# Optimization experiments

Hardware: AMD Instinct MI355X
Metric: run time of the kernel (lower is better)

## Reference

```python
import jax, jax.numpy as jnp
import numpy as np

B, T = 128, 512
H = 64          # hidden_dim
E = 64          # input_embed_dim
H4 = 4 * H


def _block_mask(in_dim, out_dim):
    # DroppedLinearV2 mask: 4 diagonal blocks, shape (4*in_dim, 4*out_dim)
    m = np.zeros((4 * in_dim, 4 * out_dim), dtype=np.float32)
    for i in range(4):
        m[i * in_dim:(i + 1) * in_dim, i * out_dim:(i + 1) * out_dim] = 1.0
    return jnp.asarray(m)


def setup_inputs() -> dict:
    key = jax.random.key(0)
    ks = jax.random.split(key, 16)
    s = 0.05
    return {
        "event": jax.random.randint(ks[0], (B, T), 0, 4),
        "time_step": jax.random.uniform(ks[1], (B, T), dtype=jnp.float32),
        "mkt_state": jax.random.randint(ks[2], (B, T), 0, 3),
        # type embedding MLP: Linear(4,E), Tanh, Linear(E,E), Tanh
        "et_W1": jax.random.normal(ks[3], (E, 4), dtype=jnp.float32) * s,
        "et_b1": jnp.zeros((E,), jnp.float32),
        "et_W2": jax.random.normal(ks[4], (E, E), dtype=jnp.float32) * s,
        "et_b2": jnp.zeros((E,), jnp.float32),
        # state embedding MLP: Linear(3,E), Tanh, Linear(E,E), Tanh
        "es_W1": jax.random.normal(ks[5], (E, 3), dtype=jnp.float32) * s,
        "es_b1": jnp.zeros((E,), jnp.float32),
        "es_W2": jax.random.normal(ks[6], (E, E), dtype=jnp.float32) * s,
        "es_b2": jnp.zeros((E,), jnp.float32),
        # 7 gates: [input_g, forget_g, output_g, input_target, forget_target, z_gate, decay]
        "g_W1": jax.random.normal(ks[7], (7, H4, E + H4), dtype=jnp.float32) * s,
        "g_b1": jnp.zeros((7, H4), jnp.float32),
        "g_W2": jax.random.normal(ks[8], (7, H4, H4), dtype=jnp.float32) * s,
        "g_b2": jnp.zeros((7, H4), jnp.float32),
        # intensity layer: DroppedLinearV2(H, 1) -> weight (4, 4H)
        "i_W": jax.random.normal(ks[9], (4, H4), dtype=jnp.float32) * s,
        "i_b": jnp.zeros((4,), jnp.float32),
    }


def _forward(event, time_step, mkt_state, et_W1, et_b1, et_W2, et_b2,
             es_W1, es_b1, es_W2, es_b2, g_W1, g_b1, g_W2, g_b2, i_W, i_b):
    seq_len = event.shape[1]
    # embeddings (mkt_state=True path): x = type_embedding + state_embedding
    oh_e = jax.nn.one_hot(event, 4, dtype=jnp.float32)
    te = jnp.tanh(jnp.tanh(oh_e @ et_W1.T + et_b1) @ et_W2.T + et_b2)
    oh_s = jax.nn.one_hot(mkt_state, 3, dtype=jnp.float32)
    se = jnp.tanh(jnp.tanh(oh_s @ es_W1.T + es_b1) @ es_W2.T + es_b2)
    x = te + se                                   # [B, T, E]

    gmask = _block_mask(H, H)                     # (4H, 4H)
    g_W2m = g_W2 * gmask.T[None]                  # effective masked gate weights
    i_Wm = i_W * _block_mask(H, 1).T              # (4, 4H)

    x_seq = jnp.swapaxes(x[:, :seq_len - 1], 0, 1)   # [T-1, B, E]
    dt_seq = time_step[:, 1:].T                      # [T-1, B]

    def step(carry, inp):
        h, c, ct = carry
        x_t, dt = inp
        v = jnp.concatenate([x_t, h], axis=1)                      # [B, E+4H]
        pre = jnp.tanh(jnp.einsum('bi,kgi->bkg', v, g_W1) + g_b1)  # [B,7,4H]
        g = jnp.einsum('bkg,kog->bko', pre, g_W2m) + g_b2          # [B,7,4H]
        inpt = jax.nn.sigmoid(g[:, 0])
        forget = jax.nn.sigmoid(g[:, 1])
        outp = jax.nn.sigmoid(g[:, 2])
        in_tg = jax.nn.sigmoid(g[:, 3])
        fg_tg = jax.nn.sigmoid(g[:, 4])
        z = jnp.tanh(g[:, 5])
        decay = jax.nn.softplus(g[:, 6])
        c_i = forget * c + inpt * z
        ct_new = fg_tg * ct + in_tg * z
        c_new = ct_new + (c_i - ct_new) * jnp.exp(-decay * dt[:, None])
        h_new = outp * jnp.tanh(c_new)
        return (h_new, c_new, ct_new), (c_i, ct_new, outp, decay, h_new)

    zero = jnp.zeros((event.shape[0], H4), jnp.float32)
    _, (cells, cell_targets, outputs, decays, h_all) = jax.lax.scan(
        step, (zero, zero, zero), (x_seq, dt_seq))

    intens = jax.nn.softplus(jnp.einsum('tbg,og->tbo', h_all, i_Wm) + i_b)
    tr = lambda a: jnp.swapaxes(a, 0, 1)  # [T-1,B,.] -> [B,T-1,.]
    return (tr(intens), tr(cells), tr(cell_targets), tr(outputs), tr(decays))


def reference(event, time_step, mkt_state, et_W1, et_b1, et_W2, et_b2,
              es_W1, es_b1, es_W2, es_b2, g_W1, g_b1, g_W2, g_b2, i_W, i_b):
    return _forward(event, time_step, mkt_state, et_W1, et_b1, et_W2, et_b2,
                    es_W1, es_b1, es_W2, es_b2, g_W1, g_b1, g_W2, g_b2, i_W, i_b)
```

## Files before the change

### kernel.cpp

```cpp
#include <hip/hip_runtime.h>
#include <stdint.h>

typedef unsigned short u16;
typedef unsigned char u8;
typedef unsigned long long u64;
typedef short s16x8 __attribute__((ext_vector_type(8)));
typedef float f32x4 __attribute__((ext_vector_type(4)));
typedef float f32x2 __attribute__((ext_vector_type(2)));
typedef unsigned int u32x4 __attribute__((ext_vector_type(4)));
typedef unsigned int u32x2 __attribute__((ext_vector_type(2)));

#define NB 128
#define NT 512
#define NH 256
#define GQ 8
#define MBQ 16
#define STEPS 511

#define WS_HBUF 0
#define WS_X12  131072
#define WS_BAR  134144

#define OFF_H     0
#define OFF_PRE   8448
#define OFF_G     24576
#define OFF_XC    55040
#define OFF_B2    78336
#define OFF_IW    80128
#define OFF_X12   80384
#define OFF_IDXA  83456
#define OFF_DTA   91648
#define SMEM_BYTES 124416

__device__ __forceinline__ u16 f2bf(float f) {
  unsigned u = __float_as_uint(f);
  u += 0x7FFFu + ((u >> 16) & 1u);
  return (u16)(u >> 16);
}
__device__ __forceinline__ float sigm(float x) { return 1.0f / (1.0f + __expf(-x)); }
__device__ __forceinline__ float tanh_fast(float x) {
  float e = __expf(2.0f * x);
  return 1.0f - 2.0f / (e + 1.0f);
}
__device__ __forceinline__ float softplus_f(float x) {
  return fmaxf(x, 0.0f) + __logf(1.0f + __expf(-fabsf(x)));
}

__global__ void ct4_prep(const float* __restrict__ etW1, const float* __restrict__ etb1,
                         const float* __restrict__ etW2, const float* __restrict__ etb2,
                         const float* __restrict__ esW1, const float* __restrict__ esb1,
                         const float* __restrict__ esW2, const float* __restrict__ esb2,
                         char* __restrict__ ws) {
  __shared__ float sT[4][64];
  __shared__ float sS[3][64];
  const int i = threadIdx.x;
  #pragma unroll
  for (int e = 0; e < 4; ++e) sT[e][i] = tanhf(etW1[i * 4 + e] + etb1[i]);
  #pragma unroll
  for (int s = 0; s < 3; ++s) sS[s][i] = tanhf(esW1[i * 3 + s] + esb1[i]);
  __syncthreads();
  float te[4], se[3];
  #pragma unroll
  for (int e = 0; e < 4; ++e) {
    float a = etb2[i];
    for (int jj = 0; jj < 64; ++jj) a += sT[e][jj] * etW2[i * 64 + jj];
    te[e] = tanhf(a);
  }
  #pragma unroll
  for (int s = 0; s < 3; ++s) {
    float a = esb2[i];
    for (int jj = 0; jj < 64; ++jj) a += sS[s][jj] * esW2[i * 64 + jj];
    se[s] = tanhf(a);
  }
  float* x12 = (float*)(ws + WS_X12);
  #pragma unroll
  for (int e = 0; e < 4; ++e)
    #pragma unroll
    for (int s = 0; s < 3; ++s) x12[(e * 3 + s) * 64 + i] = te[e] + se[s];
  u32x4* hz = (u32x4*)(ws + WS_HBUF);
  u32x4 z = {0u, 0u, 0u, 0u};
  for (int p = i; p < 65536 / 16; p += 64) hz[p] = z;
  int* bars = (int*)(ws + WS_BAR);
  for (int p = i; p < 1024; p += 64) bars[p] = 0;
}

__global__ __launch_bounds__(512, 1) void ct4_main(
    const int* __restrict__ ev, const float* __restrict__ ts, const int* __restrict__ mk,
    const float* __restrict__ gW1, const float* __restrict__ gb1,
    const float* __restrict__ gW2, const float* __restrict__ gb2,
    const float* __restrict__ iW, const float* __restrict__ ibp,
    float* __restrict__ out, char* __restrict__ ws) {
  extern __shared__ char smem[];
  u16* h_lds = (u16*)(smem + OFF_H);
  float* g_lds = (float*)(smem + OFF_G);
  float* xc_lds = (float*)(smem + OFF_XC);
  float* b2_lds = (float*)(smem + OFF_B2);
  float* iw_lds = (float*)(smem + OFF_IW);
  float* x12_lds = (float*)(smem + OFF_X12);
  u8* idx_all = (u8*)(smem + OFF_IDXA);
  float* dt_all = (float*)(smem + OFF_DTA);

  const int tid = threadIdx.x;
  const int bid = blockIdx.x;
  const int grp = bid & 7;
  const int j = bid >> 3;
  const int b0 = grp * MBQ;
  const int wave = tid >> 6;
  const int q = (tid >> 4) & 3;
  const int c = tid & 15;
  const int kloc0 = 2 * j;

  u16* hbuf = (u16*)(ws + WS_HBUF);
  int* bars = (int*)(ws + WS_BAR);
  int* myflag = bars + grp * 128 + j * 32;

  for (int p = tid; p < 12 * 64; p += 512) x12_lds[p] = ((const float*)(ws + WS_X12))[p];
  for (int p = tid; p < 16 * 264 / 2; p += 512) ((unsigned*)h_lds)[p] = 0u;
  if (tid < 448) {
    int kk = tid >> 6, o = tid & 63;
    b2_lds[kk * 64 + o] = gb2[kk * 256 + j * 64 + o];
  }
  if (tid < 64) iw_lds[tid] = iW[j * 256 + j * 64 + tid];
  const float ibj = ibp[j];
  for (int p = tid; p < STEPS * 16; p += 512) {
    int t = p >> 4, b = p & 15;
    idx_all[p] = (u8)(ev[(b0 + b) * NT + t] * 3 + mk[(b0 + b) * NT + t]);
    dt_all[p] = ts[(b0 + b) * NT + t + 1];
  }
  __syncthreads();
  if (tid < 448) {
    int kk = tid >> 6, o = tid & 63;
    const float* row = gW1 + (size_t)(kk * 256 + j * 64 + o) * 320;
    float a[12];
    float bb = gb1[kk * 256 + j * 64 + o];
    #pragma unroll
    for (int m = 0; m < 12; ++m) a[m] = bb;
    for (int i = 0; i < 64; ++i) {
      float w = row[i];
      #pragma unroll
      for (int m = 0; m < 12; ++m) a[m] += x12_lds[m * 64 + i] * w;
    }
    #pragma unroll
    for (int m = 0; m < 12; ++m) xc_lds[(kk * 64 + o) * 13 + m] = a[m];
  }

  s16x8 a1[4][8];
  s16x8 a2[4][2];
  const int k = wave;
  if (wave < 7) {
    #pragma unroll
    for (int s = 0; s < 8; ++s) {
      int kt = (s < 6) ? (s + (s >= kloc0 ? 2 : 0)) : (kloc0 + (s - 6));
      #pragma unroll
      for (int mt = 0; mt < 4; ++mt) {
        const float* p = gW1 + (size_t)(k * 256 + j * 64 + 16 * mt + c) * 320 + 64 + 32 * kt + 8 * q;
        union { s16x8 v; u16 u[8]; } fr;
        #pragma unroll
        for (int i = 0; i < 8; ++i) fr.u[i] = f2bf(p[i]);
        a1[mt][s] = fr.v;
      }
    }
    #pragma unroll
    for (int mt = 0; mt < 4; ++mt)
      #pragma unroll
      for (int kt = 0; kt < 2; ++kt) {
        const float* p = gW2 + (size_t)(k * 256 + j * 64 + 16 * mt + c) * 256 + j * 64 + 32 * kt + 8 * q;
        union { s16x8 v; u16 u[8]; } fr;
        #pragma unroll
        for (int i = 0; i < 8; ++i) fr.u[i] = f2bf(p[i]);
        a2[mt][kt] = fr.v;
      }
  }

  float ccA[2] = {0.f, 0.f};
  float cctA[2] = {0.f, 0.f};
  f32x4 acc[4] = {};
  const f32x4 fzero = {};
  __syncthreads();

  const int O_CELL = NB * STEPS * 4;
  const int SZB = NB * STEPS * NH;
  const int O_CT = O_CELL + SZB;
  const int O_OUT = O_CT + SZB;
  const int O_DEC = O_OUT + SZB;

  for (int t = 0; t < STEPS; ++t) {
    if (wave < 7) {
      #pragma unroll
      for (int s = 0; s < 6; ++s) {
        int ks = s + (s >= kloc0 ? 2 : 0);
        s16x8 bf = *(const s16x8*)&h_lds[c * 264 + 32 * ks + 8 * q];
        #pragma unroll
        for (int mt = 0; mt < 4; ++mt)
          acc[mt] = __builtin_amdgcn_mfma_f32_16x16x32_bf16(a1[mt][s], bf, acc[mt], 0, 0, 0);
      }
      u16* preW = (u16*)(smem + OFF_PRE) + k * (16 * 72);
      int midx = (int)idx_all[t * 16 + c];
      #pragma unroll
      for (int mt = 0; mt < 4; ++mt) {
        int o = 16 * mt + 4 * q;
        const float* xr = &xc_lds[(k * 64 + o) * 13 + midx];
        u16 u0 = f2bf(tanh_fast(acc[mt][0] + xr[0]));
        u16 u1 = f2bf(tanh_fast(acc[mt][1] + xr[13]));
        u16 u2 = f2bf(tanh_fast(acc[mt][2] + xr[26]));
        u16 u3 = f2bf(tanh_fast(acc[mt][3] + xr[39]));
        u32x2 pk;
        pk[0] = (unsigned)u0 | ((unsigned)u1 << 16);
        pk[1] = (unsigned)u2 | ((unsigned)u3 << 16);
        *(u32x2*)&preW[c * 72 + o] = pk;
      }
      f32x4 acc2[4] = {};
      #pragma unroll
      for (int kt = 0; kt < 2; ++kt) {
        s16x8 pf = *(const s16x8*)&preW[c * 72 + 32 * kt + 8 * q];
        #pragma unroll
        for (int mt = 0; mt < 4; ++mt)
          acc2[mt] = __builtin_amdgcn_mfma_f32_16x16x32_bf16(a2[mt][kt], pf, acc2[mt], 0, 0, 0);
      }
      #pragma unroll
      for (int mt = 0; mt < 4; ++mt)
        *(f32x4*)&g_lds[(k * 16 + c) * 68 + 16 * mt + 4 * q] = acc2[mt];
    }
    __syncthreads();

    const int b = tid >> 5, o2 = (tid & 31) * 2;
    float ip = 0.f;
    float ci[2], ctn[2], opv[2], dcv[2];
    {
      float dtv = dt_all[t * 16 + b];
      float G[7][2];
      #pragma unroll
      for (int kk = 0; kk < 7; ++kk) {
        f32x2 gg = *(const f32x2*)&g_lds[(kk * 16 + b) * 68 + o2];
        G[kk][0] = gg[0] + b2_lds[kk * 64 + o2];
        G[kk][1] = gg[1] + b2_lds[kk * 64 + o2 + 1];
      }
      float hnv[2];
      #pragma unroll
      for (int e = 0; e < 2; ++e) {
        float inp = sigm(G[0][e]);
        float fg = sigm(G[1][e]);
        float op = sigm(G[2][e]);
        float itg = sigm(G[3][e]);
        float ftg = sigm(G[4][e]);
        float z = tanh_fast(G[5][e]);
        float dc = softplus_f(G[6][e]);
        float c_i = fg * ccA[e] + inp * z;
        float c_t = ftg * cctA[e] + itg * z;
        float edv = __expf(-dc * dtv);
        float c_n = c_t + (c_i - c_t) * edv;
        float h_n = op * tanh_fast(c_n);
        ccA[e] = c_n;
        cctA[e] = c_t;
        ci[e] = c_i; ctn[e] = c_t; opv[e] = op; dcv[e] = dc;
        hnv[e] = h_n;
        ip += iw_lds[o2 + e] * h_n;
      }
      unsigned hp = (unsigned)f2bf(hnv[0]) | ((unsigned)f2bf(hnv[1]) << 16);
      if (t < STEPS - 1) {
        *(unsigned*)&h_lds[b * 264 + j * 64 + o2] = hp;
        __hip_atomic_store((unsigned*)&hbuf[((size_t)(((t + 1) & 1) * GQ + grp) * MBQ + b) * 256 + j * 64 + o2],
                           hp, __ATOMIC_RELAXED, __HIP_MEMORY_SCOPE_AGENT);
      }
    }
    __syncthreads();

    auto C2 = [&]() {
      size_t base = ((size_t)(b0 + b) * STEPS + t) * NH + j * 64 + o2;
      f32x2 v;
      v[0] = ci[0];  v[1] = ci[1];  __builtin_nontemporal_store(v, (f32x2*)&out[O_CELL + base]);
      v[0] = ctn[0]; v[1] = ctn[1]; __builtin_nontemporal_store(v, (f32x2*)&out[O_CT + base]);
      v[0] = opv[0]; v[1] = opv[1]; __builtin_nontemporal_store(v, (f32x2*)&out[O_OUT + base]);
      v[0] = dcv[0]; v[1] = dcv[1]; __builtin_nontemporal_store(v, (f32x2*)&out[O_DEC + base]);
      #pragma unroll
      for (int d = 1; d < 32; d <<= 1) ip += __shfl_xor(ip, d, 32);
      if ((tid & 31) == 0)
        __builtin_nontemporal_store(softplus_f(ip + ibj),
                                    &out[((size_t)(b0 + b) * STEPS + t) * 4 + j]);
    };

    if (t < STEPS - 1) {
      if (tid == 0) __hip_atomic_store(myflag, t + 1, __ATOMIC_RELAXED, __HIP_MEMORY_SCOPE_AGENT);
      if (wave < 7) {
        #pragma unroll
        for (int mt = 0; mt < 4; ++mt) acc[mt] = fzero;
        #pragma unroll
        for (int s = 6; s < 8; ++s) {
          int ks = kloc0 + (s - 6);
          s16x8 bf = *(const s16x8*)&h_lds[c * 264 + 32 * ks + 8 * q];
          #pragma unroll
          for (int mt = 0; mt < 4; ++mt)
            acc[mt] = __builtin_amdgcn_mfma_f32_16x16x32_bf16(a1[mt][s], bf, acc[mt], 0, 0, 0);
        }
        C2();
      } else {
        C2();
        const int l = tid & 63;
        const int row = l >> 2;
        const int segb = (l & 3) * 32;
        int* f0p = bars + grp * 128 + (0 + (0 >= j)) * 32;
        int* f1p = bars + grp * 128 + (1 + (1 >= j)) * 32;
        int* f2p = bars + grp * 128 + (2 + (2 >= j)) * 32;
        for (;;) {
          int f0 = __hip_atomic_load(f0p, __ATOMIC_RELAXED, __HIP_MEMORY_SCOPE_AGENT);
          int f1 = __hip_atomic_load(f1p, __ATOMIC_RELAXED, __HIP_MEMORY_SCOPE_AGENT);
          int f2 = __hip_atomic_load(f2p, __ATOMIC_RELAXED, __HIP_MEMORY_SCOPE_AGENT);
          if (f0 > t && f1 > t && f2 > t) break;
          __builtin_amdgcn_s_sleep(1);
        }
        const char* rbase = (const char*)hbuf +
            ((size_t)(((t + 1) & 1) * GQ + grp) * MBQ + row) * 512 + segb;
        u64 dv[3][4];
        #pragma unroll
        for (int rb = 0; rb < 3; ++rb) {
          int jr = rb + (rb >= j);
          const u64* src = (const u64*)(rbase + jr * 128);
          #pragma unroll
          for (int kq = 0; kq < 4; ++kq)
            dv[rb][kq] = __hip_atomic_load(src + kq, __ATOMIC_RELAXED, __HIP_MEMORY_SCOPE_AGENT);
        }
        char* lbase = (char*)h_lds + row * 528 + segb;
        #pragma unroll
        for (int rb = 0; rb < 3; ++rb) {
          int jr = rb + (rb >= j);
          #pragma unroll
          for (int kq = 0; kq < 4; ++kq)
            *(u64*)(lbase + jr * 128 + 8 * kq) = dv[rb][kq];
        }
      }
      __syncthreads();
    } else {
      C2();
    }
  }
}

extern "C" void kernel_launch(void* const* d_in, const int* in_sizes, int n_in,
                              void* d_out, int out_size, void* d_ws, size_t ws_size,
                              hipStream_t stream) {
  const int* ev = (const int*)d_in[0];
  const float* ts = (const float*)d_in[1];
  const int* mk = (const int*)d_in[2];
  const float* etW1 = (const float*)d_in[3];
  const float* etb1 = (const float*)d_in[4];
  const float* etW2 = (const float*)d_in[5];
  const float* etb2 = (const float*)d_in[6];
  const float* esW1 = (const float*)d_in[7];
  const float* esb1 = (const float*)d_in[8];
  const float* esW2 = (const float*)d_in[9];
  const float* esb2 = (const float*)d_in[10];
  const float* gW1 = (const float*)d_in[11];
  const float* gb1 = (const float*)d_in[12];
  const float* gW2 = (const float*)d_in[13];
  const float* gb2 = (const float*)d_in[14];
  const float* iW = (const float*)d_in[15];
  const float* ibv = (const float*)d_in[16];
  char* ws = (char*)d_ws;
  float* out = (float*)d_out;

  ct4_prep<<<1, 64, 0, stream>>>(etW1, etb1, etW2, etb2, esW1, esb1, esW2, esb2, ws);
  (void)hipFuncSetAttribute((const void*)ct4_main,
                            hipFuncAttributeMaxDynamicSharedMemorySize, SMEM_BYTES);
  ct4_main<<<GQ * 4, 512, SMEM_BYTES, stream>>>(ev, ts, mk, gW1, gb1, gW2, gb2, iW, ibv, out, ws);
}
```

Measured before the change: 2.230 ms.

## Halve block to 256 threads, each wave computing two gates

The main kernel drops from 8 waves to 4 per block. Each wave now holds the bf16 weight fragments for two of the seven gates, reusing one set of h-fragment loads for both gates' MFMAs. The elementwise cell update handles 4 hidden units per thread and writes wider vector stores, and wave 3 now does the cross-block polling and gather. This cuts block-wide barrier cost and redundant LDS reads, but doubles per-wave register pressure for weights and serialises two gates' MFMA chains per wave.

```diff
diff --git a/kernel.cpp b/kernel.cpp
--- a/kernel.cpp
+++ b/kernel.cpp
@@ -84,7 +84,7 @@
   for (int p = i; p < 1024; p += 64) bars[p] = 0;
 }
 
-__global__ __launch_bounds__(512, 1) void ct4_main(
+__global__ __launch_bounds__(256, 1) void ct4_main(
     const int* __restrict__ ev, const float* __restrict__ ts, const int* __restrict__ mk,
     const float* __restrict__ gW1, const float* __restrict__ gb1,
     const float* __restrict__ gW2, const float* __restrict__ gb2,
@@ -114,22 +114,22 @@
   int* bars = (int*)(ws + WS_BAR);
   int* myflag = bars + grp * 128 + j * 32;
 
-  for (int p = tid; p < 12 * 64; p += 512) x12_lds[p] = ((const float*)(ws + WS_X12))[p];
-  for (int p = tid; p < 16 * 264 / 2; p += 512) ((unsigned*)h_lds)[p] = 0u;
-  if (tid < 448) {
-    int kk = tid >> 6, o = tid & 63;
+  for (int p = tid; p < 12 * 64; p += 256) x12_lds[p] = ((const float*)(ws + WS_X12))[p];
+  for (int p = tid; p < 16 * 264 / 2; p += 256) ((unsigned*)h_lds)[p] = 0u;
+  for (int p = tid; p < 448; p += 256) {
+    int kk = p >> 6, o = p & 63;
     b2_lds[kk * 64 + o] = gb2[kk * 256 + j * 64 + o];
   }
   if (tid < 64) iw_lds[tid] = iW[j * 256 + j * 64 + tid];
   const float ibj = ibp[j];
-  for (int p = tid; p < STEPS * 16; p += 512) {
+  for (int p = tid; p < STEPS * 16; p += 256) {
     int t = p >> 4, b = p & 15;
     idx_all[p] = (u8)(ev[(b0 + b) * NT + t] * 3 + mk[(b0 + b) * NT + t]);
     dt_all[p] = ts[(b0 + b) * NT + t + 1];
   }
   __syncthreads();
-  if (tid < 448) {
-    int kk = tid >> 6, o = tid & 63;
+  for (int r = tid; r < 448; r += 256) {
+    int kk = r >> 6, o = r & 63;
     const float* row = gW1 + (size_t)(kk * 256 + j * 64 + o) * 320;
     float a[12];
     float bb = gb1[kk * 256 + j * 64 + o];
@@ -144,37 +144,40 @@
     for (int m = 0; m < 12; ++m) xc_lds[(kk * 64 + o) * 13 + m] = a[m];
   }
 
-  s16x8 a1[4][8];
-  s16x8 a2[4][2];
-  const int k = wave;
-  if (wave < 7) {
-    #pragma unroll
-    for (int s = 0; s < 8; ++s) {
-      int kt = (s < 6) ? (s + (s >= kloc0 ? 2 : 0)) : (kloc0 + (s - 6));
-      #pragma unroll
-      for (int mt = 0; mt < 4; ++mt) {
-        const float* p = gW1 + (size_t)(k * 256 + j * 64 + 16 * mt + c) * 320 + 64 + 32 * kt + 8 * q;
-        union { s16x8 v; u16 u[8]; } fr;
-        #pragma unroll
-        for (int i = 0; i < 8; ++i) fr.u[i] = f2bf(p[i]);
-        a1[mt][s] = fr.v;
-      }
-    }
-    #pragma unroll
-    for (int mt = 0; mt < 4; ++mt)
-      #pragma unroll
-      for (int kt = 0; kt < 2; ++kt) {
-        const float* p = gW2 + (size_t)(k * 256 + j * 64 + 16 * mt + c) * 256 + j * 64 + 32 * kt + 8 * q;
-        union { s16x8 v; u16 u[8]; } fr;
-        #pragma unroll
-        for (int i = 0; i < 8; ++i) fr.u[i] = f2bf(p[i]);
-        a2[mt][kt] = fr.v;
-      }
-  }
-
-  float ccA[2] = {0.f, 0.f};
-  float cctA[2] = {0.f, 0.f};
-  f32x4 acc[4] = {};
+  s16x8 a1[2][4][8];
+  s16x8 a2[2][4][2];
+  #pragma unroll
+  for (int gg = 0; gg < 2; ++gg) {
+    const int k = 2 * wave + gg;
+    if (k < 7) {
+      #pragma unroll
+      for (int s = 0; s < 8; ++s) {
+        int kt = (s < 6) ? (s + (s >= kloc0 ? 2 : 0)) : (kloc0 + (s - 6));
+        #pragma unroll
+        for (int mt = 0; mt < 4; ++mt) {
+          const float* p = gW1 + (size_t)(k * 256 + j * 64 + 16 * mt + c) * 320 + 64 + 32 * kt + 8 * q;
+          union { s16x8 v; u16 u[8]; } fr;
+          #pragma unroll
+          for (int i = 0; i < 8; ++i) fr.u[i] = f2bf(p[i]);
+          a1[gg][mt][s] = fr.v;
+        }
+      }
+      #pragma unroll
+      for (int mt = 0; mt < 4; ++mt)
+        #pragma unroll
+        for (int kt = 0; kt < 2; ++kt) {
+          const float* p = gW2 + (size_t)(k * 256 + j * 64 + 16 * mt + c) * 256 + j * 64 + 32 * kt + 8 * q;
+          union { s16x8 v; u16 u[8]; } fr;
+          #pragma unroll
+          for (int i = 0; i < 8; ++i) fr.u[i] = f2bf(p[i]);
+          a2[gg][mt][kt] = fr.v;
+        }
+    }
+  }
+
+  float ccA[4] = {0.f, 0.f, 0.f, 0.f};
+  float cctA[4] = {0.f, 0.f, 0.f, 0.f};
+  f32x4 acc[2][4] = {};
   const f32x4 fzero = {};
   __syncthreads();
 
@@ -185,59 +188,68 @@
   const int O_DEC = O_OUT + SZB;
 
   for (int t = 0; t < STEPS; ++t) {
-    if (wave < 7) {
+    {
+      s16x8 bfr[6];
       #pragma unroll
       for (int s = 0; s < 6; ++s) {
         int ks = s + (s >= kloc0 ? 2 : 0);
-        s16x8 bf = *(const s16x8*)&h_lds[c * 264 + 32 * ks + 8 * q];
-        #pragma unroll
-        for (int mt = 0; mt < 4; ++mt)
-          acc[mt] = __builtin_amdgcn_mfma_f32_16x16x32_bf16(a1[mt][s], bf, acc[mt], 0, 0, 0);
-      }
-      u16* preW = (u16*)(smem + OFF_PRE) + k * (16 * 72);
+        bfr[s] = *(const s16x8*)&h_lds[c * 264 + 32 * ks + 8 * q];
+      }
       int midx = (int)idx_all[t * 16 + c];
       #pragma unroll
-      for (int mt = 0; mt < 4; ++mt) {
-        int o = 16 * mt + 4 * q;
-        const float* xr = &xc_lds[(k * 64 + o) * 13 + midx];
-        u16 u0 = f2bf(tanh_fast(acc[mt][0] + xr[0]));
-        u16 u1 = f2bf(tanh_fast(acc[mt][1] + xr[13]));
-        u16 u2 = f2bf(tanh_fast(acc[mt][2] + xr[26]));
-        u16 u3 = f2bf(tanh_fast(acc[mt][3] + xr[39]));
-        u32x2 pk;
-        pk[0] = (unsigned)u0 | ((unsigned)u1 << 16);
-        pk[1] = (unsigned)u2 | ((unsigned)u3 << 16);
-        *(u32x2*)&preW[c * 72 + o] = pk;
-      }
-      f32x4 acc2[4] = {};
-      #pragma unroll
-      for (int kt = 0; kt < 2; ++kt) {
-        s16x8 pf = *(const s16x8*)&preW[c * 72 + 32 * kt + 8 * q];
-        #pragma unroll
-        for (int mt = 0; mt < 4; ++mt)
-          acc2[mt] = __builtin_amdgcn_mfma_f32_16x16x32_bf16(a2[mt][kt], pf, acc2[mt], 0, 0, 0);
-      }
-      #pragma unroll
-      for (int mt = 0; mt < 4; ++mt)
-        *(f32x4*)&g_lds[(k * 16 + c) * 68 + 16 * mt + 4 * q] = acc2[mt];
+      for (int gg = 0; gg < 2; ++gg) {
+        const int k = 2 * wave + gg;
+        if (k < 7) {
+          #pragma unroll
+          for (int s = 0; s < 6; ++s)
+            #pragma unroll
+            for (int mt = 0; mt < 4; ++mt)
+              acc[gg][mt] = __builtin_amdgcn_mfma_f32_16x16x32_bf16(a1[gg][mt][s], bfr[s], acc[gg][mt], 0, 0, 0);
+          u16* preW = (u16*)(smem + OFF_PRE) + k * (16 * 72);
+          #pragma unroll
+          for (int mt = 0; mt < 4; ++mt) {
+            int o = 16 * mt + 4 * q;
+            const float* xr = &xc_lds[(k * 64 + o) * 13 + midx];
+            u16 u0 = f2bf(tanh_fast(acc[gg][mt][0] + xr[0]));
+            u16 u1 = f2bf(tanh_fast(acc[gg][mt][1] + xr[13]));
+            u16 u2 = f2bf(tanh_fast(acc[gg][mt][2] + xr[26]));
+            u16 u3 = f2bf(tanh_fast(acc[gg][mt][3] + xr[39]));
+            u32x2 pk;
+            pk[0] = (unsigned)u0 | ((unsigned)u1 << 16);
+            pk[1] = (unsigned)u2 | ((unsigned)u3 << 16);
+            *(u32x2*)&preW[c * 72 + o] = pk;
+          }
+          f32x4 acc2[4] = {};
+          #pragma unroll
+          for (int kt = 0; kt < 2; ++kt) {
+            s16x8 pf = *(const s16x8*)&preW[c * 72 + 32 * kt + 8 * q];
+            #pragma unroll
+            for (int mt = 0; mt < 4; ++mt)
+              acc2[mt] = __builtin_amdgcn_mfma_f32_16x16x32_bf16(a2[gg][mt][kt], pf, acc2[mt], 0, 0, 0);
+          }
+          #pragma unroll
+          for (int mt = 0; mt < 4; ++mt)
+            *(f32x4*)&g_lds[(k * 16 + c) * 68 + 16 * mt + 4 * q] = acc2[mt];
+        }
+      }
     }
     __syncthreads();
 
-    const int b = tid >> 5, o2 = (tid & 31) * 2;
+    const int b = tid >> 4, o4 = (tid & 15) * 4;
     float ip = 0.f;
-    float ci[2], ctn[2], opv[2], dcv[2];
+    float ci[4], ctn[4], opv[4], dcv[4];
     {
       float dtv = dt_all[t * 16 + b];
-      float G[7][2];
+      float G[7][4];
       #pragma unroll
       for (int kk = 0; kk < 7; ++kk) {
-        f32x2 gg = *(const f32x2*)&g_lds[(kk * 16 + b) * 68 + o2];
-        G[kk][0] = gg[0] + b2_lds[kk * 64 + o2];
-        G[kk][1] = gg[1] + b2_lds[kk * 64 + o2 + 1];
-      }
-      float hnv[2];
-      #pragma unroll
-      for (int e = 0; e < 2; ++e) {
+        f32x4 gg4 = *(const f32x4*)&g_lds[(kk * 16 + b) * 68 + o4];
+        #pragma unroll
+        for (int e = 0; e < 4; ++e) G[kk][e] = gg4[e] + b2_lds[kk * 64 + o4 + e];
+      }
+      float hnv[4];
+      #pragma unroll
+      for (int e = 0; e < 4; ++e) {
         float inp = sigm(G[0][e]);
         float fg = sigm(G[1][e]);
         float op = sigm(G[2][e]);
@@ -254,47 +266,63 @@
         cctA[e] = c_t;
         ci[e] = c_i; ctn[e] = c_t; opv[e] = op; dcv[e] = dc;
         hnv[e] = h_n;
-        ip += iw_lds[o2 + e] * h_n;
-      }
-      unsigned hp = (unsigned)f2bf(hnv[0]) | ((unsigned)f2bf(hnv[1]) << 16);
+        ip += iw_lds[o4 + e] * h_n;
+      }
       if (t < STEPS - 1) {
-        *(unsigned*)&h_lds[b * 264 + j * 64 + o2] = hp;
-        __hip_atomic_store((unsigned*)&hbuf[((size_t)(((t + 1) & 1) * GQ + grp) * MBQ + b) * 256 + j * 64 + o2],
+        u64 hp = (u64)f2bf(hnv[0]) | ((u64)f2bf(hnv[1]) << 16) |
+                 ((u64)f2bf(hnv[2]) << 32) | ((u64)f2bf(hnv[3]) << 48);
+        *(u64*)&h_lds[b * 264 + j * 64 + o4] = hp;
+        __hip_atomic_store((u64*)&hbuf[((size_t)(((t + 1) & 1) * GQ + grp) * MBQ + b) * 256 + j * 64 + o4],
                            hp, __ATOMIC_RELAXED, __HIP_MEMORY_SCOPE_AGENT);
       }
     }
     __syncthreads();
 
     auto C2 = [&]() {
-      size_t base = ((size_t)(b0 + b) * STEPS + t) * NH + j * 64 + o2;
-      f32x2 v;
-      v[0] = ci[0];  v[1] = ci[1];  __builtin_nontemporal_store(v, (f32x2*)&out[O_CELL + base]);
-      v[0] = ctn[0]; v[1] = ctn[1]; __builtin_nontemporal_store(v, (f32x2*)&out[O_CT + base]);
-      v[0] = opv[0]; v[1] = opv[1]; __builtin_nontemporal_store(v, (f32x2*)&out[O_OUT + base]);
-      v[0] = dcv[0]; v[1] = dcv[1]; __builtin_nontemporal_store(v, (f32x2*)&out[O_DEC + base]);
-      #pragma unroll
-      for (int d = 1; d < 32; d <<= 1) ip += __shfl_xor(ip, d, 32);
-      if ((tid & 31) == 0)
+      size_t base = ((size_t)(b0 + b) * STEPS + t) * NH + j * 64 + o4;
+      f32x4 v;
+      #pragma unroll
+      for (int e = 0; e < 4; ++e) v[e] = ci[e];
+      __builtin_nontemporal_store(v, (f32x4*)&out[O_CELL + base]);
+      #pragma unroll
+      for (int e = 0; e < 4; ++e) v[e] = ctn[e];
+      __builtin_nontemporal_store(v, (f32x4*)&out[O_CT + base]);
+      #pragma unroll
+      for (int e = 0; e < 4; ++e) v[e] = opv[e];
+      __builtin_nontemporal_store(v, (f32x4*)&out[O_OUT + base]);
+      #pragma unroll
+      for (int e = 0; e < 4; ++e) v[e] = dcv[e];
+      __builtin_nontemporal_store(v, (f32x4*)&out[O_DEC + base]);
+      #pragma unroll
+      for (int d = 1; d < 16; d <<= 1) ip += __shfl_xor(ip, d, 16);
+      if ((tid & 15) == 0)
         __builtin_nontemporal_store(softplus_f(ip + ibj),
                                     &out[((size_t)(b0 + b) * STEPS + t) * 4 + j]);
     };
 
     if (t < STEPS - 1) {
       if (tid == 0) __hip_atomic_store(myflag, t + 1, __ATOMIC_RELAXED, __HIP_MEMORY_SCOPE_AGENT);
-      if (wave < 7) {
-        #pragma unroll
-        for (int mt = 0; mt < 4; ++mt) acc[mt] = fzero;
-        #pragma unroll
-        for (int s = 6; s < 8; ++s) {
-          int ks = kloc0 + (s - 6);
-          s16x8 bf = *(const s16x8*)&h_lds[c * 264 + 32 * ks + 8 * q];
-          #pragma unroll
-          for (int mt = 0; mt < 4; ++mt)
-            acc[mt] = __builtin_amdgcn_mfma_f32_16x16x32_bf16(a1[mt][s], bf, acc[mt], 0, 0, 0);
-        }
-        C2();
-      } else {
-        C2();
+      {
+        s16x8 bfl[2];
+        #pragma unroll
+        for (int sl = 0; sl < 2; ++sl)
+          bfl[sl] = *(const s16x8*)&h_lds[c * 264 + 32 * (kloc0 + sl) + 8 * q];
+        #pragma unroll
+        for (int gg = 0; gg < 2; ++gg) {
+          const int k = 2 * wave + gg;
+          if (k < 7) {
+            #pragma unroll
+            for (int mt = 0; mt < 4; ++mt) acc[gg][mt] = fzero;
+            #pragma unroll
+            for (int sl = 0; sl < 2; ++sl)
+              #pragma unroll
+              for (int mt = 0; mt < 4; ++mt)
+                acc[gg][mt] = __builtin_amdgcn_mfma_f32_16x16x32_bf16(a1[gg][mt][6 + sl], bfl[sl], acc[gg][mt], 0, 0, 0);
+          }
+        }
+      }
+      C2();
+      if (wave == 3) {
         const int l = tid & 63;
         const int row = l >> 2;
         const int segb = (l & 3) * 32;
@@ -361,5 +389,5 @@
   ct4_prep<<<1, 64, 0, stream>>>(etW1, etb1, etW2, etb2, esW1, esb1, esW2, esb2, ws);
   (void)hipFuncSetAttribute((const void*)ct4_main,
                             hipFuncAttributeMaxDynamicSharedMemorySize, SMEM_BYTES);
-  ct4_main<<<GQ * 4, 512, SMEM_BYTES, stream>>>(ev, ts, mk, gW1, gb1, gW2, gb2, iW, ibv, out, ws);
-}
+  ct4_main<<<GQ * 4, 256, SMEM_BYTES, stream>>>(ev, ts, mk, gW1, gb1, gW2, gb2, iW, ibv, out, ws);
+}
```

After: 2.876 ms. 28.9% more time.

## Load remote hidden state directly into MFMA registers, dropping second block barrier

Applied to the files above, without the earlier changes.

Each compute wave now polls the peer flags itself and loads the remote blocks' hidden-state slices from the global exchange buffer straight into B-operand registers. The dedicated loader wave no longer stages them through LDS, so the second __syncthreads per timestep disappears. The LDS hidden buffer shrinks to the block's own 64-column slice. This shortens the serial per-step critical path, at the cost of seven waves each polling flags and issuing redundant global atomic loads for the same data.

```diff
diff --git a/kernel.cpp b/kernel.cpp
--- a/kernel.cpp
+++ b/kernel.cpp
@@ -22,15 +22,15 @@
 #define WS_BAR  134144
 
 #define OFF_H     0
-#define OFF_PRE   8448
-#define OFF_G     24576
-#define OFF_XC    55040
-#define OFF_B2    78336
-#define OFF_IW    80128
-#define OFF_X12   80384
-#define OFF_IDXA  83456
-#define OFF_DTA   91648
-#define SMEM_BYTES 124416
+#define OFF_PRE   2304
+#define OFF_G     18432
+#define OFF_XC    48896
+#define OFF_B2    72192
+#define OFF_IW    73984
+#define OFF_X12   74240
+#define OFF_IDXA  77312
+#define OFF_DTA   85504
+#define SMEM_BYTES 118208
 
 __device__ __forceinline__ u16 f2bf(float f) {
   unsigned u = __float_as_uint(f);
@@ -44,6 +44,12 @@
 }
 __device__ __forceinline__ float softplus_f(float x) {
   return fmaxf(x, 0.0f) + __logf(1.0f + __expf(-fabsf(x)));
+}
+__device__ __forceinline__ int ald(const int* p) {
+  return __hip_atomic_load(p, __ATOMIC_RELAXED, __HIP_MEMORY_SCOPE_AGENT);
+}
+__device__ __forceinline__ u64 ald64(const u64* p) {
+  return __hip_atomic_load(p, __ATOMIC_RELAXED, __HIP_MEMORY_SCOPE_AGENT);
 }
 
 __global__ void ct4_prep(const float* __restrict__ etW1, const float* __restrict__ etb1,
@@ -109,13 +115,17 @@
   const int q = (tid >> 4) & 3;
   const int c = tid & 15;
   const int kloc0 = 2 * j;
+  const int k = wave;
 
   u16* hbuf = (u16*)(ws + WS_HBUF);
   int* bars = (int*)(ws + WS_BAR);
   int* myflag = bars + grp * 128 + j * 32;
+  int* f0p = bars + grp * 128 + (0 + (0 >= j)) * 32;
+  int* f1p = bars + grp * 128 + (1 + (1 >= j)) * 32;
+  int* f2p = bars + grp * 128 + (2 + (2 >= j)) * 32;
 
   for (int p = tid; p < 12 * 64; p += 512) x12_lds[p] = ((const float*)(ws + WS_X12))[p];
-  for (int p = tid; p < 16 * 264 / 2; p += 512) ((unsigned*)h_lds)[p] = 0u;
+  for (int p = tid; p < 16 * 72 * 2 / 4; p += 512) ((unsigned*)h_lds)[p] = 0u;
   if (tid < 448) {
     int kk = tid >> 6, o = tid & 63;
     b2_lds[kk * 64 + o] = gb2[kk * 256 + j * 64 + o];
@@ -146,7 +156,6 @@
 
   s16x8 a1[4][8];
   s16x8 a2[4][2];
-  const int k = wave;
   if (wave < 7) {
     #pragma unroll
     for (int s = 0; s < 8; ++s) {
@@ -175,6 +184,10 @@
   float ccA[2] = {0.f, 0.f};
   float cctA[2] = {0.f, 0.f};
   f32x4 acc[4] = {};
+  union RB { s16x8 v; u64 d[2]; };
+  RB rbf[6];
+  #pragma unroll
+  for (int s = 0; s < 6; ++s) { rbf[s].d[0] = 0ull; rbf[s].d[1] = 0ull; }
   const f32x4 fzero = {};
   __syncthreads();
 
@@ -187,13 +200,10 @@
   for (int t = 0; t < STEPS; ++t) {
     if (wave < 7) {
       #pragma unroll
-      for (int s = 0; s < 6; ++s) {
-        int ks = s + (s >= kloc0 ? 2 : 0);
-        s16x8 bf = *(const s16x8*)&h_lds[c * 264 + 32 * ks + 8 * q];
+      for (int s = 0; s < 6; ++s)
         #pragma unroll
         for (int mt = 0; mt < 4; ++mt)
-          acc[mt] = __builtin_amdgcn_mfma_f32_16x16x32_bf16(a1[mt][s], bf, acc[mt], 0, 0, 0);
-      }
+          acc[mt] = __builtin_amdgcn_mfma_f32_16x16x32_bf16(a1[mt][s], rbf[s].v, acc[mt], 0, 0, 0);
       u16* preW = (u16*)(smem + OFF_PRE) + k * (16 * 72);
       int midx = (int)idx_all[t * 16 + c];
       #pragma unroll
@@ -256,16 +266,58 @@
         hnv[e] = h_n;
         ip += iw_lds[o2 + e] * h_n;
       }
-      unsigned hp = (unsigned)f2bf(hnv[0]) | ((unsigned)f2bf(hnv[1]) << 16);
       if (t < STEPS - 1) {
-        *(unsigned*)&h_lds[b * 264 + j * 64 + o2] = hp;
+        unsigned hp = (unsigned)f2bf(hnv[0]) | ((unsigned)f2bf(hnv[1]) << 16);
+        *(unsigned*)&h_lds[b * 72 + o2] = hp;
         __hip_atomic_store((unsigned*)&hbuf[((size_t)(((t + 1) & 1) * GQ + grp) * MBQ + b) * 256 + j * 64 + o2],
                            hp, __ATOMIC_RELAXED, __HIP_MEMORY_SCOPE_AGENT);
       }
     }
     __syncthreads();
 
-    auto C2 = [&]() {
+    if (tid == 0 && t < STEPS - 1)
+      __hip_atomic_store(myflag, t + 1, __ATOMIC_RELAXED, __HIP_MEMORY_SCOPE_AGENT);
+
+    if (t < STEPS - 1) {
+      if (wave < 7) {
+        s16x8 bfl0 = *(const s16x8*)&h_lds[c * 72 + 8 * q];
+        s16x8 bfl1 = *(const s16x8*)&h_lds[c * 72 + 32 + 8 * q];
+        #pragma unroll
+        for (int mt = 0; mt < 4; ++mt)
+          acc[mt] = __builtin_amdgcn_mfma_f32_16x16x32_bf16(a1[mt][6], bfl0, fzero, 0, 0, 0);
+        #pragma unroll
+        for (int mt = 0; mt < 4; ++mt)
+          acc[mt] = __builtin_amdgcn_mfma_f32_16x16x32_bf16(a1[mt][7], bfl1, acc[mt], 0, 0, 0);
+      }
+      {
+        size_t base = ((size_t)(b0 + b) * STEPS + t) * NH + j * 64 + o2;
+        f32x2 v;
+        v[0] = ci[0];  v[1] = ci[1];  __builtin_nontemporal_store(v, (f32x2*)&out[O_CELL + base]);
+        v[0] = ctn[0]; v[1] = ctn[1]; __builtin_nontemporal_store(v, (f32x2*)&out[O_CT + base]);
+        v[0] = opv[0]; v[1] = opv[1]; __builtin_nontemporal_store(v, (f32x2*)&out[O_OUT + base]);
+        v[0] = dcv[0]; v[1] = dcv[1]; __builtin_nontemporal_store(v, (f32x2*)&out[O_DEC + base]);
+        #pragma unroll
+        for (int d = 1; d < 32; d <<= 1) ip += __shfl_xor(ip, d, 32);
+        if ((tid & 31) == 0)
+          __builtin_nontemporal_store(softplus_f(ip + ibj),
+                                      &out[((size_t)(b0 + b) * STEPS + t) * 4 + j]);
+      }
+      if (wave < 7) {
+        for (;;) {
+          int f0 = ald(f0p), f1 = ald(f1p), f2 = ald(f2p);
+          if (f0 > t && f1 > t && f2 > t) break;
+          __builtin_amdgcn_s_sleep(1);
+        }
+        const u16* hb = hbuf + ((size_t)(((t + 1) & 1) * GQ + grp) * MBQ + c) * 256 + 8 * q;
+        #pragma unroll
+        for (int s = 0; s < 6; ++s) {
+          int ks = s + (s >= kloc0 ? 2 : 0);
+          const u64* src = (const u64*)(hb + ks * 32);
+          rbf[s].d[0] = ald64(src);
+          rbf[s].d[1] = ald64(src + 1);
+        }
+      }
+    } else {
       size_t base = ((size_t)(b0 + b) * STEPS + t) * NH + j * 64 + o2;
       f32x2 v;
       v[0] = ci[0];  v[1] = ci[1];  __builtin_nontemporal_store(v, (f32x2*)&out[O_CELL + base]);
@@ -277,60 +329,6 @@
       if ((tid & 31) == 0)
         __builtin_nontemporal_store(softplus_f(ip + ibj),
                                     &out[((size_t)(b0 + b) * STEPS + t) * 4 + j]);
-    };
-
-    if (t < STEPS - 1) {
-      if (tid == 0) __hip_atomic_store(myflag, t + 1, __ATOMIC_RELAXED, __HIP_MEMORY_SCOPE_AGENT);
-      if (wave < 7) {
-        #pragma unroll
-        for (int mt = 0; mt < 4; ++mt) acc[mt] = fzero;
-        #pragma unroll
-        for (int s = 6; s < 8; ++s) {
-          int ks = kloc0 + (s - 6);
-          s16x8 bf = *(const s16x8*)&h_lds[c * 264 + 32 * ks + 8 * q];
-          #pragma unroll
-          for (int mt = 0; mt < 4; ++mt)
-            acc[mt] = __builtin_amdgcn_mfma_f32_16x16x32_bf16(a1[mt][s], bf, acc[mt], 0, 0, 0);
-        }
-        C2();
-      } else {
-        C2();
-        const int l = tid & 63;
-        const int row = l >> 2;
-        const int segb = (l & 3) * 32;
-        int* f0p = bars + grp * 128 + (0 + (0 >= j)) * 32;
-        int* f1p = bars + grp * 128 + (1 + (1 >= j)) * 32;
-        int* f2p = bars + grp * 128 + (2 + (2 >= j)) * 32;
-        for (;;) {
-          int f0 = __hip_atomic_load(f0p, __ATOMIC_RELAXED, __HIP_MEMORY_SCOPE_AGENT);
-          int f1 = __hip_atomic_load(f1p, __ATOMIC_RELAXED, __HIP_MEMORY_SCOPE_AGENT);
-          int f2 = __hip_atomic_load(f2p, __ATOMIC_RELAXED, __HIP_MEMORY_SCOPE_AGENT);
-          if (f0 > t && f1 > t && f2 > t) break;
-          __builtin_amdgcn_s_sleep(1);
-        }
-        const char* rbase = (const char*)hbuf +
-            ((size_t)(((t + 1) & 1) * GQ + grp) * MBQ + row) * 512 + segb;
-        u64 dv[3][4];
-        #pragma unroll
-        for (int rb = 0; rb < 3; ++rb) {
-          int jr = rb + (rb >= j);
-          const u64* src = (const u64*)(rbase + jr * 128);
-          #pragma unroll
-          for (int kq = 0; kq < 4; ++kq)
-            dv[rb][kq] = __hip_atomic_load(src + kq, __ATOMIC_RELAXED, __HIP_MEMORY_SCOPE_AGENT);
-        }
-        char* lbase = (char*)h_lds + row * 528 + segb;
-        #pragma unroll
-        for (int rb = 0; rb < 3; ++rb) {
-          int jr = rb + (rb >= j);
-          #pragma unroll
-          for (int kq = 0; kq < 4; ++kq)
-            *(u64*)(lbase + jr * 128 + 8 * kq) = dv[rb][kq];
-        }
-      }
-      __syncthreads();
-    } else {
-      C2();
     }
   }
 }
```

Measured after the change: 3.286 ms. 1.47x slower.
